# Performance work log

Measured on AMD Instinct MI355X. Metric: run time of the kernel, lower is better.

Reference implementation:

```python
import jax, jax.numpy as jnp
import numpy as np

N = 50000
E = 400000
IN_DIM = 128
HID = 128
OUT = 128
HEADS = 8
NEG_SLOPE = 0.2  # PyG GATConv default
BN_EPS = 1e-5


def _gat_conv(x, W, a_src, a_dst, b, src, dst, concat):
    """PyG GATConv (eval): self-loops added by caller. x:[N,F], W:[F,H*C], a_*:[H,C]."""
    H, C = a_src.shape
    xW = (x @ W).reshape(N, H, C)                       # [N,H,C]
    es = jnp.sum(xW * a_src[None], axis=-1)             # [N,H]
    ed = jnp.sum(xW * a_dst[None], axis=-1)             # [N,H]
    e = jax.nn.leaky_relu(es[src] + ed[dst], NEG_SLOPE) # [E,H]
    m = jax.ops.segment_max(e, dst, num_segments=N)     # softmax over incoming edges per dst
    ex = jnp.exp(e - m[dst])
    denom = jax.ops.segment_sum(ex, dst, num_segments=N)
    alpha = ex / denom[dst]                             # [E,H]
    out = jax.ops.segment_sum(xW[src] * alpha[:, :, None], dst, num_segments=N)  # [N,H,C]
    out = out.reshape(N, H * C) if concat else out.mean(axis=1)
    return out + b


def _bn_eval(h, g, be, rm, rv):
    return (h - rm) * jax.lax.rsqrt(rv + BN_EPS) * g + be


def setup_inputs() -> dict:
    key = jax.random.key(0)
    ks = jax.random.split(key, 20)
    C1 = HID // HEADS
    f32 = jnp.float32
    inp = {
        "x": jax.random.normal(ks[0], (N, IN_DIM), dtype=f32),
        "edge_index": jax.random.randint(ks[1], (2, E), 0, N, dtype=jnp.int64),
        # GAT layer 1 (in->hid, 8 heads, concat)
        "W1": jax.random.normal(ks[2], (IN_DIM, HEADS * C1), dtype=f32) * 0.05,
        "a_src1": jax.random.normal(ks[3], (HEADS, C1), dtype=f32) * 0.05,
        "a_dst1": jax.random.normal(ks[4], (HEADS, C1), dtype=f32) * 0.05,
        "b1": jnp.zeros((HEADS * C1,), dtype=f32),
        # GAT layer 2 (hid->hid, 8 heads, concat)
        "W2": jax.random.normal(ks[5], (HID, HEADS * C1), dtype=f32) * 0.05,
        "a_src2": jax.random.normal(ks[6], (HEADS, C1), dtype=f32) * 0.05,
        "a_dst2": jax.random.normal(ks[7], (HEADS, C1), dtype=f32) * 0.05,
        "b2": jnp.zeros((HEADS * C1,), dtype=f32),
        # GAT layer 3 (hid->out, 1 head, no concat)
        "W3": jax.random.normal(ks[8], (HID, OUT), dtype=f32) * 0.05,
        "a_src3": jax.random.normal(ks[9], (1, OUT), dtype=f32) * 0.05,
        "a_dst3": jax.random.normal(ks[10], (1, OUT), dtype=f32) * 0.05,
        "b3": jnp.zeros((OUT,), dtype=f32),
        # residual linears
        "R1w": jax.random.normal(ks[11], (IN_DIM, HID), dtype=f32) * 0.05,
        "R1b": jnp.zeros((HID,), dtype=f32),
        "R2w": jax.random.normal(ks[12], (HID, HID), dtype=f32) * 0.05,
        "R2b": jnp.zeros((HID,), dtype=f32),
        "R3w": jax.random.normal(ks[13], (HID, OUT), dtype=f32) * 0.05,
        "R3b": jnp.zeros((OUT,), dtype=f32),
        # batch norms (eval mode: running stats)
        "g1": jnp.ones((HID,), dtype=f32), "be1": jnp.zeros((HID,), dtype=f32),
        "rm1": jnp.zeros((HID,), dtype=f32), "rv1": jnp.ones((HID,), dtype=f32),
        "g2": jnp.ones((HID,), dtype=f32), "be2": jnp.zeros((HID,), dtype=f32),
        "rm2": jnp.zeros((HID,), dtype=f32), "rv2": jnp.ones((HID,), dtype=f32),
    }
    return inp


def reference(x, edge_index, W1, a_src1, a_dst1, b1, W2, a_src2, a_dst2, b2,
              W3, a_src3, a_dst3, b3, R1w, R1b, R2w, R2b, R3w, R3b,
              g1, be1, rm1, rv1, g2, be2, rm2, rv2):
    # PyG GATConv adds self-loops by default
    loops = jnp.arange(N, dtype=edge_index.dtype)
    src = jnp.concatenate([edge_index[0], loops])
    dst = jnp.concatenate([edge_index[1], loops])

    h = _gat_conv(x, W1, a_src1, a_dst1, b1, src, dst, concat=True) + (x @ R1w + R1b)
    h1 = jax.nn.relu(_bn_eval(h, g1, be1, rm1, rv1))  # dropout identity in eval

    h = _gat_conv(h1, W2, a_src2, a_dst2, b2, src, dst, concat=True) + (h1 @ R2w + R2b)
    h2 = jax.nn.relu(_bn_eval(h, g2, be2, rm2, rv2))

    out = _gat_conv(h2, W3, a_src3, a_dst3, b3, src, dst, concat=False) + (h2 @ R3w + R3b)
    return out
```

## Files before the change

kernel.cpp:

```cpp
#include <hip/hip_runtime.h>
#include <hip/hip_bf16.h>
#include <type_traits>

typedef __hip_bfloat16 bf16;
typedef __hip_bfloat162 bf162;
typedef short v8s __attribute__((ext_vector_type(8)));
typedef float v4f __attribute__((ext_vector_type(4)));

__device__ __forceinline__ float lrelu(float x) { return x > 0.f ? x : 0.2f * x; }
__device__ __forceinline__ float b2f(bf16 v) { return __bfloat162float(v); }

__global__ void k_count(const int* __restrict__ ei, int* __restrict__ cnt, int E) {
    int i = blockIdx.x * 256 + threadIdx.x;
    if (i < E) atomicAdd(&cnt[ei[E + i]], 1);
}

__global__ void k_scan1(const int* __restrict__ cnt, int* __restrict__ ofs,
                        int* __restrict__ bsum, int n) {
    __shared__ int sh[256];
    int t = threadIdx.x;
    int base = blockIdx.x * 1024 + t * 4;
    int v[4]; int s = 0;
#pragma unroll
    for (int i = 0; i < 4; ++i) { v[i] = (base + i < n) ? cnt[base + i] : 0; s += v[i]; }
    sh[t] = s; __syncthreads();
    for (int o = 1; o < 256; o <<= 1) {
        int x = 0; if (t >= o) x = sh[t - o];
        __syncthreads();
        sh[t] += x;
        __syncthreads();
    }
    int excl = sh[t] - s;
#pragma unroll
    for (int i = 0; i < 4; ++i) { if (base + i < n) ofs[base + i] = excl; excl += v[i]; }
    if (t == 255) bsum[blockIdx.x] = sh[255];
}

__global__ void k_scan2(const int* __restrict__ bsum, int* __restrict__ bpre, int nb) {
    int l = threadIdx.x;
    int v = (l < nb) ? bsum[l] : 0;
    int orig = v;
    for (int o = 1; o < 64; o <<= 1) {
        int x = __shfl_up(v, o);
        if (l >= o) v += x;
    }
    if (l < nb) bpre[l] = v - orig;
}

__global__ void k_scan3(int* __restrict__ ofs, int* __restrict__ cur,
                        const int* __restrict__ bpre, int n) {
    int i = blockIdx.x * 256 + threadIdx.x;
    if (i < n) { int v = ofs[i] + bpre[i >> 10]; ofs[i] = v; cur[i] = v; }
}

__global__ void k_fill(const int* __restrict__ ei, int* __restrict__ cur,
                       int* __restrict__ csr, int E) {
    int i = blockIdx.x * 256 + threadIdx.x;
    if (i < E) {
        int d = ei[E + i];
        int pos = atomicAdd(&cur[d], 1);
        csr[pos] = ei[i];
    }
}

__global__ void k_transpose(const float* __restrict__ s0, const float* __restrict__ s1,
                            const float* __restrict__ s2, const float* __restrict__ s3,
                            const float* __restrict__ s4, const float* __restrict__ s5,
                            bf16* __restrict__ wt) {
    const float* src;
    switch (blockIdx.x) {
        case 0: src = s0; break; case 1: src = s1; break; case 2: src = s2; break;
        case 3: src = s3; break; case 4: src = s4; break; default: src = s5; break;
    }
    bf16* dst = wt + blockIdx.x * 16384;
    for (int i = threadIdx.x; i < 16384; i += 256) {
        int k = i >> 7, n = i & 127;
        dst[n * 128 + k] = __float2bfloat16(src[i]);
    }
}

__global__ void k_params(const float* b1, const float* R1b, const float* g1, const float* be1,
                         const float* rm1, const float* rv1,
                         const float* b2, const float* R2b, const float* g2, const float* be2,
                         const float* rm2, const float* rv2,
                         const float* b3, const float* R3b, float* __restrict__ prm) {
    int c = threadIdx.x;
    if (c < 128) {
        float s1 = g1[c] * rsqrtf(rv1[c] + 1e-5f);
        prm[c]       = b1[c] + R1b[c];
        prm[128 + c] = s1;
        prm[256 + c] = be1[c] - rm1[c] * s1;
        float s2 = g2[c] * rsqrtf(rv2[c] + 1e-5f);
        prm[384 + c] = b2[c] + R2b[c];
        prm[512 + c] = s2;
        prm[640 + c] = be2[c] - rm2[c] * s2;
        prm[768 + c] = b3[c] + R3b[c];
    }
}

template <typename T>
__global__ void gemm_dual(const T* __restrict__ A,
                          const bf16* __restrict__ BT0, const bf16* __restrict__ BT1,
                          bf16* __restrict__ O0, bf16* __restrict__ O1, int nrows) {
    __shared__ bf16 Ash[128 * 128];
    __shared__ bf16 Bsh[128 * 128];
    const bf16* BT = (blockIdx.y == 0) ? BT0 : BT1;
    bf16* O = (blockIdx.y == 0) ? O0 : O1;
    const int t = threadIdx.x;
    const int rowbase = blockIdx.x * 128;
    {
        const int r = t >> 1, hf = t & 1;
        int gr = rowbase + r; if (gr >= nrows) gr = nrows - 1;
        const float4* bsrc = (const float4*)(BT + r * 128 + hf * 64);
        if constexpr (std::is_same<T, float>::value) {
            const float4* asrc = (const float4*)(A + (size_t)gr * 128 + hf * 64);
#pragma unroll
            for (int j = 0; j < 8; ++j) {
                float4 u = asrc[2 * j], w = asrc[2 * j + 1];
                union { bf16 h[8]; float4 f; } tmp;
                tmp.h[0] = __float2bfloat16(u.x); tmp.h[1] = __float2bfloat16(u.y);
                tmp.h[2] = __float2bfloat16(u.z); tmp.h[3] = __float2bfloat16(u.w);
                tmp.h[4] = __float2bfloat16(w.x); tmp.h[5] = __float2bfloat16(w.y);
                tmp.h[6] = __float2bfloat16(w.z); tmp.h[7] = __float2bfloat16(w.w);
                int c = hf * 8 + j, cp = c ^ (r & 7);
                *(float4*)(&Ash[r * 128 + cp * 8]) = tmp.f;
                *(float4*)(&Bsh[r * 128 + cp * 8]) = bsrc[j];
            }
        } else {
            const float4* asrc = (const float4*)(A + (size_t)gr * 128 + hf * 64);
#pragma unroll
            for (int j = 0; j < 8; ++j) {
                int c = hf * 8 + j, cp = c ^ (r & 7);
                *(float4*)(&Ash[r * 128 + cp * 8]) = asrc[j];
                *(float4*)(&Bsh[r * 128 + cp * 8]) = bsrc[j];
            }
        }
    }
    __syncthreads();
    const int wave = t >> 6, lane = t & 63, quad = lane >> 4, l16 = lane & 15;
    v4f acc[2][8];
#pragma unroll
    for (int i = 0; i < 2; ++i)
#pragma unroll
        for (int j = 0; j < 8; ++j) acc[i][j] = (v4f){0.f, 0.f, 0.f, 0.f};
#pragma unroll
    for (int kit = 0; kit < 4; ++kit) {
        v8s afr[2], bfr[8];
#pragma unroll
        for (int rt = 0; rt < 2; ++rt) {
            int row = wave * 32 + rt * 16 + l16;
            int cp = (kit * 4 + quad) ^ (row & 7);
            afr[rt] = *(const v8s*)(&Ash[row * 128 + cp * 8]);
        }
#pragma unroll
        for (int ct = 0; ct < 8; ++ct) {
            int nn = ct * 16 + l16;
            int cp = (kit * 4 + quad) ^ (nn & 7);
            bfr[ct] = *(const v8s*)(&Bsh[nn * 128 + cp * 8]);
        }
#pragma unroll
        for (int rt = 0; rt < 2; ++rt)
#pragma unroll
            for (int ct = 0; ct < 8; ++ct)
                acc[rt][ct] = __builtin_amdgcn_mfma_f32_16x16x32_bf16(afr[rt], bfr[ct], acc[rt][ct], 0, 0, 0);
    }
#pragma unroll
    for (int rt = 0; rt < 2; ++rt)
#pragma unroll
        for (int ct = 0; ct < 8; ++ct)
#pragma unroll
            for (int r = 0; r < 4; ++r) {
                int gr = rowbase + wave * 32 + rt * 16 + quad * 4 + r;
                if (gr < nrows) O[(size_t)gr * 128 + ct * 16 + l16] = __float2bfloat16(acc[rt][ct][r]);
            }
}

__global__ void k_prep8(const bf16* __restrict__ xW, const float* __restrict__ asrc,
                        const float* __restrict__ adst,
                        float* __restrict__ es, float* __restrict__ ed, int n) {
    int wave = threadIdx.x >> 6, lane = threadIdx.x & 63;
    int node = blockIdx.x * 4 + wave;
    if (node >= n) return;
    bf162 xp = *(const bf162*)(xW + (size_t)node * 128 + 2 * lane);
    float2 sp = *(const float2*)(asrc + 2 * lane);
    float2 dp = *(const float2*)(adst + 2 * lane);
    float x0 = b2f(xp.x), x1 = b2f(xp.y);
    float ps = x0 * sp.x + x1 * sp.y;
    float pd = x0 * dp.x + x1 * dp.y;
    for (int o = 1; o < 8; o <<= 1) { ps += __shfl_xor(ps, o); pd += __shfl_xor(pd, o); }
    if ((lane & 7) == 0) {
        int h = lane >> 3;
        es[node * 8 + h] = ps;
        ed[node * 8 + h] = pd;
    }
}

__global__ void k_prep1(const bf16* __restrict__ xW, const float* __restrict__ asrc,
                        const float* __restrict__ adst,
                        float* __restrict__ es, float* __restrict__ ed, int n) {
    int wave = threadIdx.x >> 6, lane = threadIdx.x & 63;
    int node = blockIdx.x * 4 + wave;
    if (node >= n) return;
    bf162 xp = *(const bf162*)(xW + (size_t)node * 128 + 2 * lane);
    float2 sp = *(const float2*)(asrc + 2 * lane);
    float2 dp = *(const float2*)(adst + 2 * lane);
    float x0 = b2f(xp.x), x1 = b2f(xp.y);
    float ps = x0 * sp.x + x1 * sp.y;
    float pd = x0 * dp.x + x1 * dp.y;
    for (int o = 1; o < 64; o <<= 1) { ps += __shfl_xor(ps, o); pd += __shfl_xor(pd, o); }
    if (lane == 0) { es[node] = ps; ed[node] = pd; }
}

__global__ void k_agg8(const bf16* __restrict__ xW, const float* __restrict__ es,
                       const float* __restrict__ ed,
                       const int* __restrict__ ofs, const int* __restrict__ cur,
                       const int* __restrict__ csr,
                       const bf16* __restrict__ rres, const float* __restrict__ prm,
                       bf16* __restrict__ hout, int n) {
    int wave = threadIdx.x >> 6, lane = threadIdx.x & 63;
    int node = blockIdx.x * 4 + wave;
    if (node >= n) return;
    const int g = lane >> 4, l16 = lane & 15;
    const int c0 = l16 * 8;
    const int h = l16 >> 1;
    float edv = ed[node * 8 + h];
    int beg = ofs[node], end = cur[node];
    float acc[8];
    float den = 0.f;
#pragma unroll
    for (int i = 0; i < 8; ++i) acc[i] = 0.f;
    if (g == 0) {
        float ws = __expf(lrelu(es[node * 8 + h] + edv));
        v8s xv = *(const v8s*)(xW + (size_t)node * 128 + c0);
        const bf16* xb = (const bf16*)&xv;
        den = ws;
#pragma unroll
        for (int i = 0; i < 8; ++i) acc[i] = ws * b2f(xb[i]);
    }
    for (int base = beg; base < end; base += 64) {
        int m = end - base; if (m > 64) m = 64;
        int idx = (lane < m) ? csr[base + lane] : node;
        for (int j = 0; j < m; j += 4) {
            int s = __shfl(idx, j + g);
            float e = es[s * 8 + h];
            v8s xv = *(const v8s*)(xW + (size_t)s * 128 + c0);
            float w = ((j + g) < m) ? __expf(lrelu(e + edv)) : 0.f;
            const bf16* xb = (const bf16*)&xv;
            den += w;
#pragma unroll
            for (int i = 0; i < 8; ++i) acc[i] += w * b2f(xb[i]);
        }
    }
    den += __shfl_xor(den, 16); den += __shfl_xor(den, 32);
#pragma unroll
    for (int i = 0; i < 8; ++i) {
        acc[i] += __shfl_xor(acc[i], 16);
        acc[i] += __shfl_xor(acc[i], 32);
    }
    if (g == 0) {
        float inv = 1.f / den;
        v8s rv = *(const v8s*)(rres + (size_t)node * 128 + c0);
        const bf16* rb = (const bf16*)&rv;
        bf16 outv[8];
#pragma unroll
        for (int i = 0; i < 8; ++i) {
            int c = c0 + i;
            float v = acc[i] * inv + prm[c] + b2f(rb[i]);
            v = fmaxf(v * prm[128 + c] + prm[256 + c], 0.f);
            outv[i] = __float2bfloat16(v);
        }
        *(v8s*)(hout + (size_t)node * 128 + c0) = *(v8s*)outv;
    }
}

__global__ void k_agg1(const bf16* __restrict__ xW, const float* __restrict__ es,
                       const float* __restrict__ ed,
                       const int* __restrict__ ofs, const int* __restrict__ cur,
                       const int* __restrict__ csr,
                       const bf16* __restrict__ rres, const float* __restrict__ bias,
                       float* __restrict__ out, int n) {
    int wave = threadIdx.x >> 6, lane = threadIdx.x & 63;
    int node = blockIdx.x * 4 + wave;
    if (node >= n) return;
    const int g = lane >> 4, l16 = lane & 15;
    const int c0 = l16 * 8;
    float edv = ed[node];
    int beg = ofs[node], end = cur[node];
    float acc[8];
    float den = 0.f;
#pragma unroll
    for (int i = 0; i < 8; ++i) acc[i] = 0.f;
    if (g == 0) {
        float ws = __expf(lrelu(es[node] + edv));
        v8s xv = *(const v8s*)(xW + (size_t)node * 128 + c0);
        const bf16* xb = (const bf16*)&xv;
        den = ws;
#pragma unroll
        for (int i = 0; i < 8; ++i) acc[i] = ws * b2f(xb[i]);
    }
    for (int base = beg; base < end; base += 64) {
        int m = end - base; if (m > 64) m = 64;
        int idx = (lane < m) ? csr[base + lane] : node;
        for (int j = 0; j < m; j += 4) {
            int s = __shfl(idx, j + g);
            float e = es[s];
            v8s xv = *(const v8s*)(xW + (size_t)s * 128 + c0);
            float w = ((j + g) < m) ? __expf(lrelu(e + edv)) : 0.f;
            const bf16* xb = (const bf16*)&xv;
            den += w;
#pragma unroll
            for (int i = 0; i < 8; ++i) acc[i] += w * b2f(xb[i]);
        }
    }
    den += __shfl_xor(den, 16); den += __shfl_xor(den, 32);
#pragma unroll
    for (int i = 0; i < 8; ++i) {
        acc[i] += __shfl_xor(acc[i], 16);
        acc[i] += __shfl_xor(acc[i], 32);
    }
    if (g == 0) {
        float inv = 1.f / den;
        v8s rv = *(const v8s*)(rres + (size_t)node * 128 + c0);
        const bf16* rb = (const bf16*)&rv;
        float4 o0, o1;
        float ov[8];
#pragma unroll
        for (int i = 0; i < 8; ++i)
            ov[i] = acc[i] * inv + bias[c0 + i] + b2f(rb[i]);
        o0.x = ov[0]; o0.y = ov[1]; o0.z = ov[2]; o0.w = ov[3];
        o1.x = ov[4]; o1.y = ov[5]; o1.z = ov[6]; o1.w = ov[7];
        *(float4*)(out + (size_t)node * 128 + c0) = o0;
        *(float4*)(out + (size_t)node * 128 + c0 + 4) = o1;
    }
}

extern "C" void kernel_launch(void* const* d_in, const int* in_sizes, int n_in,
                              void* d_out, int out_size, void* d_ws, size_t ws_size,
                              hipStream_t stream) {
    const float* x   = (const float*)d_in[0];
    const int*   ei  = (const int*)d_in[1];
    const float* W1  = (const float*)d_in[2];
    const float* as1 = (const float*)d_in[3];
    const float* ad1 = (const float*)d_in[4];
    const float* b1  = (const float*)d_in[5];
    const float* W2  = (const float*)d_in[6];
    const float* as2 = (const float*)d_in[7];
    const float* ad2 = (const float*)d_in[8];
    const float* b2  = (const float*)d_in[9];
    const float* W3  = (const float*)d_in[10];
    const float* as3 = (const float*)d_in[11];
    const float* ad3 = (const float*)d_in[12];
    const float* b3  = (const float*)d_in[13];
    const float* R1w = (const float*)d_in[14];
    const float* R1b = (const float*)d_in[15];
    const float* R2w = (const float*)d_in[16];
    const float* R2b = (const float*)d_in[17];
    const float* R3w = (const float*)d_in[18];
    const float* R3b = (const float*)d_in[19];
    const float* g1  = (const float*)d_in[20];
    const float* be1 = (const float*)d_in[21];
    const float* rm1 = (const float*)d_in[22];
    const float* rv1 = (const float*)d_in[23];
    const float* g2  = (const float*)d_in[24];
    const float* be2 = (const float*)d_in[25];
    const float* rm2 = (const float*)d_in[26];
    const float* rv2 = (const float*)d_in[27];

    const int N = in_sizes[0] / 128;
    const int E = in_sizes[1] / 2;

    char* p = (char*)d_ws;
    size_t off = 0;
    auto alloc = [&](size_t b) { void* r = p + off; off = (off + b + 255) & ~(size_t)255; return r; };
    int*   cnt  = (int*)alloc((size_t)N * 4);
    int*   ofs  = (int*)alloc((size_t)N * 4);
    int*   cur  = (int*)alloc((size_t)N * 4);
    int*   bsum = (int*)alloc(64 * 4);
    int*   bpre = (int*)alloc(64 * 4);
    int*   csr  = (int*)alloc((size_t)E * 4);
    bf16*  WT   = (bf16*)alloc((size_t)6 * 16384 * 2);
    float* prm  = (float*)alloc(896 * 4);
    float* es   = (float*)alloc((size_t)N * 8 * 4);
    float* ed   = (float*)alloc((size_t)N * 8 * 4);
    bf16*  xW   = (bf16*)alloc((size_t)N * 128 * 2);
    bf16*  rres = (bf16*)alloc((size_t)N * 128 * 2);
    bf16*  hA   = (bf16*)alloc((size_t)N * 128 * 2);
    bf16*  hB   = (bf16*)alloc((size_t)N * 128 * 2);
    (void)ws_size; (void)n_in; (void)out_size;

    hipMemsetAsync(cnt, 0, (size_t)N * 4, stream);
    const int eb = (E + 255) / 256;
    const int nb = (N + 1023) / 1024;
    k_count<<<eb, 256, 0, stream>>>(ei, cnt, E);
    k_scan1<<<nb, 256, 0, stream>>>(cnt, ofs, bsum, N);
    k_scan2<<<1, 64, 0, stream>>>(bsum, bpre, nb);
    k_scan3<<<(N + 255) / 256, 256, 0, stream>>>(ofs, cur, bpre, N);
    k_fill<<<eb, 256, 0, stream>>>(ei, cur, csr, E);
    k_transpose<<<6, 256, 0, stream>>>(W1, R1w, W2, R2w, W3, R3w, WT);
    k_params<<<1, 128, 0, stream>>>(b1, R1b, g1, be1, rm1, rv1,
                                    b2, R2b, g2, be2, rm2, rv2, b3, R3b, prm);

    const int gx = (N + 127) / 128;
    const int nw = (N + 3) / 4;
    gemm_dual<float><<<dim3(gx, 2), 256, 0, stream>>>(x, WT, WT + 16384, xW, rres, N);
    k_prep8<<<nw, 256, 0, stream>>>(xW, as1, ad1, es, ed, N);
    k_agg8<<<nw, 256, 0, stream>>>(xW, es, ed, ofs, cur, csr, rres, prm, hA, N);
    gemm_dual<bf16><<<dim3(gx, 2), 256, 0, stream>>>(hA, WT + 2 * 16384, WT + 3 * 16384, xW, rres, N);
    k_prep8<<<nw, 256, 0, stream>>>(xW, as2, ad2, es, ed, N);
    k_agg8<<<nw, 256, 0, stream>>>(xW, es, ed, ofs, cur, csr, rres, prm + 384, hB, N);
    gemm_dual<bf16><<<dim3(gx, 2), 256, 0, stream>>>(hB, WT + 4 * 16384, WT + 5 * 16384, xW, rres, N);
    k_prep1<<<nw, 256, 0, stream>>>(xW, as3, ad3, es, ed, N);
    k_agg1<<<nw, 256, 0, stream>>>(xW, es, ed, ofs, cur, csr, rres, prm + 768, (float*)d_out, N);
}
```

Before: 350.2 us.

## Fold attention logits into GEMM as extra weight columns; dedupe edge exp work

```diff
diff --git a/kernel.cpp b/kernel.cpp
--- a/kernel.cpp
+++ b/kernel.cpp
@@ -63,47 +63,83 @@
     }
 }
 
-__global__ void k_transpose(const float* __restrict__ s0, const float* __restrict__ s1,
-                            const float* __restrict__ s2, const float* __restrict__ s3,
-                            const float* __restrict__ s4, const float* __restrict__ s5,
-                            bf16* __restrict__ wt) {
+__global__ void k_trans(const float* __restrict__ s0, const float* __restrict__ s1,
+                        const float* __restrict__ s2, const float* __restrict__ s3,
+                        const float* __restrict__ s4, const float* __restrict__ s5,
+                        const float* __restrict__ as1, const float* __restrict__ ad1,
+                        const float* __restrict__ as2, const float* __restrict__ ad2,
+                        const float* __restrict__ as3, const float* __restrict__ ad3,
+                        const float* b1, const float* R1b, const float* g1, const float* be1,
+                        const float* rm1, const float* rv1,
+                        const float* b2, const float* R2b, const float* g2, const float* be2,
+                        const float* rm2, const float* rv2,
+                        const float* b3, const float* R3b,
+                        bf16* __restrict__ wt, float* __restrict__ prm) {
+    int b = blockIdx.x;
+    int t = threadIdx.x;
+    if (b == 6) {
+        int c = t;
+        if (c < 128) {
+            float s1v = g1[c] * rsqrtf(rv1[c] + 1e-5f);
+            prm[c]       = b1[c] + R1b[c];
+            prm[128 + c] = s1v;
+            prm[256 + c] = be1[c] - rm1[c] * s1v;
+            float s2v = g2[c] * rsqrtf(rv2[c] + 1e-5f);
+            prm[384 + c] = b2[c] + R2b[c];
+            prm[512 + c] = s2v;
+            prm[640 + c] = be2[c] - rm2[c] * s2v;
+            prm[768 + c] = b3[c] + R3b[c];
+        }
+        return;
+    }
     const float* src;
-    switch (blockIdx.x) {
+    switch (b) {
         case 0: src = s0; break; case 1: src = s1; break; case 2: src = s2; break;
         case 3: src = s3; break; case 4: src = s4; break; default: src = s5; break;
     }
-    bf16* dst = wt + blockIdx.x * 16384;
-    for (int i = threadIdx.x; i < 16384; i += 256) {
+    bf16* dst = wt + (size_t)b * 18432;
+    for (int i = t; i < 16384; i += 256) {
         int k = i >> 7, n = i & 127;
         dst[n * 128 + k] = __float2bfloat16(src[i]);
     }
-}
-
-__global__ void k_params(const float* b1, const float* R1b, const float* g1, const float* be1,
-                         const float* rm1, const float* rv1,
-                         const float* b2, const float* R2b, const float* g2, const float* be2,
-                         const float* rm2, const float* rv2,
-                         const float* b3, const float* R3b, float* __restrict__ prm) {
-    int c = threadIdx.x;
-    if (c < 128) {
-        float s1 = g1[c] * rsqrtf(rv1[c] + 1e-5f);
-        prm[c]       = b1[c] + R1b[c];
-        prm[128 + c] = s1;
-        prm[256 + c] = be1[c] - rm1[c] * s1;
-        float s2 = g2[c] * rsqrtf(rv2[c] + 1e-5f);
-        prm[384 + c] = b2[c] + R2b[c];
-        prm[512 + c] = s2;
-        prm[640 + c] = be2[c] - rm2[c] * s2;
-        prm[768 + c] = b3[c] + R3b[c];
+    if ((b & 1) == 0) {
+        int layer = b >> 1;
+        if (layer < 2) {
+            const float* asr = (layer == 0) ? as1 : as2;
+            const float* ads = (layer == 0) ? ad1 : ad2;
+            for (int i = t; i < 2048; i += 256) {
+                int row = i >> 7, k = i & 127, h = row & 7;
+                const float* av = (row < 8) ? asr : ads;
+                float s = 0.f;
+#pragma unroll
+                for (int c = 0; c < 16; ++c) s += src[k * 128 + h * 16 + c] * av[h * 16 + c];
+                dst[(128 + row) * 128 + k] = __float2bfloat16(s);
+            }
+        } else {
+            for (int i = t; i < 2048; i += 256) {
+                int row = i >> 7, k = i & 127;
+                float s = 0.f;
+                if (row == 0 || row == 8) {
+                    const float* av = (row == 0) ? as3 : ad3;
+                    for (int c = 0; c < 128; ++c) s += src[k * 128 + c] * av[c];
+                }
+                dst[(128 + row) * 128 + k] = __float2bfloat16(s);
+            }
+        }
+    } else {
+        for (int i = t; i < 2048; i += 256)
+            dst[16384 + i] = __float2bfloat16(0.f);
     }
 }
 
 template <typename T>
 __global__ void gemm_dual(const T* __restrict__ A,
                           const bf16* __restrict__ BT0, const bf16* __restrict__ BT1,
-                          bf16* __restrict__ O0, bf16* __restrict__ O1, int nrows) {
+                          bf16* __restrict__ O0, bf16* __restrict__ O1,
+                          float* __restrict__ es, float* __restrict__ ed,
+                          int mode, int nrows) {
     __shared__ bf16 Ash[128 * 128];
-    __shared__ bf16 Bsh[128 * 128];
+    __shared__ bf16 Bsh[144 * 128];
     const bf16* BT = (blockIdx.y == 0) ? BT0 : BT1;
     bf16* O = (blockIdx.y == 0) ? O0 : O1;
     const int t = threadIdx.x;
@@ -111,7 +147,6 @@
     {
         const int r = t >> 1, hf = t & 1;
         int gr = rowbase + r; if (gr >= nrows) gr = nrows - 1;
-        const float4* bsrc = (const float4*)(BT + r * 128 + hf * 64);
         if constexpr (std::is_same<T, float>::value) {
             const float4* asrc = (const float4*)(A + (size_t)gr * 128 + hf * 64);
 #pragma unroll
@@ -124,7 +159,6 @@
                 tmp.h[6] = __float2bfloat16(w.z); tmp.h[7] = __float2bfloat16(w.w);
                 int c = hf * 8 + j, cp = c ^ (r & 7);
                 *(float4*)(&Ash[r * 128 + cp * 8]) = tmp.f;
-                *(float4*)(&Bsh[r * 128 + cp * 8]) = bsrc[j];
             }
         } else {
             const float4* asrc = (const float4*)(A + (size_t)gr * 128 + hf * 64);
@@ -132,20 +166,28 @@
             for (int j = 0; j < 8; ++j) {
                 int c = hf * 8 + j, cp = c ^ (r & 7);
                 *(float4*)(&Ash[r * 128 + cp * 8]) = asrc[j];
-                *(float4*)(&Bsh[r * 128 + cp * 8]) = bsrc[j];
-            }
+            }
+        }
+    }
+    for (int s = t; s < 288; s += 256) {
+        int r = s >> 1, hf = s & 1;
+        const float4* bsrc = (const float4*)(BT + r * 128 + hf * 64);
+#pragma unroll
+        for (int j = 0; j < 8; ++j) {
+            int c = hf * 8 + j, cp = c ^ (r & 7);
+            *(float4*)(&Bsh[r * 128 + cp * 8]) = bsrc[j];
         }
     }
     __syncthreads();
     const int wave = t >> 6, lane = t & 63, quad = lane >> 4, l16 = lane & 15;
-    v4f acc[2][8];
+    v4f acc[2][9];
 #pragma unroll
     for (int i = 0; i < 2; ++i)
 #pragma unroll
-        for (int j = 0; j < 8; ++j) acc[i][j] = (v4f){0.f, 0.f, 0.f, 0.f};
+        for (int j = 0; j < 9; ++j) acc[i][j] = (v4f){0.f, 0.f, 0.f, 0.f};
 #pragma unroll
     for (int kit = 0; kit < 4; ++kit) {
-        v8s afr[2], bfr[8];
+        v8s afr[2], bfr[9];
 #pragma unroll
         for (int rt = 0; rt < 2; ++rt) {
             int row = wave * 32 + rt * 16 + l16;
@@ -153,7 +195,7 @@
             afr[rt] = *(const v8s*)(&Ash[row * 128 + cp * 8]);
         }
 #pragma unroll
-        for (int ct = 0; ct < 8; ++ct) {
+        for (int ct = 0; ct < 9; ++ct) {
             int nn = ct * 16 + l16;
             int cp = (kit * 4 + quad) ^ (nn & 7);
             bfr[ct] = *(const v8s*)(&Bsh[nn * 128 + cp * 8]);
@@ -161,7 +203,7 @@
 #pragma unroll
         for (int rt = 0; rt < 2; ++rt)
 #pragma unroll
-            for (int ct = 0; ct < 8; ++ct)
+            for (int ct = 0; ct < 9; ++ct)
                 acc[rt][ct] = __builtin_amdgcn_mfma_f32_16x16x32_bf16(afr[rt], bfr[ct], acc[rt][ct], 0, 0, 0);
     }
 #pragma unroll
@@ -173,46 +215,28 @@
                 int gr = rowbase + wave * 32 + rt * 16 + quad * 4 + r;
                 if (gr < nrows) O[(size_t)gr * 128 + ct * 16 + l16] = __float2bfloat16(acc[rt][ct][r]);
             }
-}
-
-__global__ void k_prep8(const bf16* __restrict__ xW, const float* __restrict__ asrc,
-                        const float* __restrict__ adst,
-                        float* __restrict__ es, float* __restrict__ ed, int n) {
-    int wave = threadIdx.x >> 6, lane = threadIdx.x & 63;
-    int node = blockIdx.x * 4 + wave;
-    if (node >= n) return;
-    bf162 xp = *(const bf162*)(xW + (size_t)node * 128 + 2 * lane);
-    float2 sp = *(const float2*)(asrc + 2 * lane);
-    float2 dp = *(const float2*)(adst + 2 * lane);
-    float x0 = b2f(xp.x), x1 = b2f(xp.y);
-    float ps = x0 * sp.x + x1 * sp.y;
-    float pd = x0 * dp.x + x1 * dp.y;
-    for (int o = 1; o < 8; o <<= 1) { ps += __shfl_xor(ps, o); pd += __shfl_xor(pd, o); }
-    if ((lane & 7) == 0) {
-        int h = lane >> 3;
-        es[node * 8 + h] = ps;
-        ed[node * 8 + h] = pd;
-    }
-}
-
-__global__ void k_prep1(const bf16* __restrict__ xW, const float* __restrict__ asrc,
-                        const float* __restrict__ adst,
-                        float* __restrict__ es, float* __restrict__ ed, int n) {
-    int wave = threadIdx.x >> 6, lane = threadIdx.x & 63;
-    int node = blockIdx.x * 4 + wave;
-    if (node >= n) return;
-    bf162 xp = *(const bf162*)(xW + (size_t)node * 128 + 2 * lane);
-    float2 sp = *(const float2*)(asrc + 2 * lane);
-    float2 dp = *(const float2*)(adst + 2 * lane);
-    float x0 = b2f(xp.x), x1 = b2f(xp.y);
-    float ps = x0 * sp.x + x1 * sp.y;
-    float pd = x0 * dp.x + x1 * dp.y;
-    for (int o = 1; o < 64; o <<= 1) { ps += __shfl_xor(ps, o); pd += __shfl_xor(pd, o); }
-    if (lane == 0) { es[node] = ps; ed[node] = pd; }
-}
-
-__global__ void k_agg8(const bf16* __restrict__ xW, const float* __restrict__ es,
-                       const float* __restrict__ ed,
+    if (mode != 0 && blockIdx.y == 0) {
+#pragma unroll
+        for (int rt = 0; rt < 2; ++rt)
+#pragma unroll
+            for (int r = 0; r < 4; ++r) {
+                int gr = rowbase + wave * 32 + rt * 16 + quad * 4 + r;
+                if (gr < nrows) {
+                    float v = acc[rt][8][r];
+                    if (mode == 1) {
+                        if (l16 < 8) es[(size_t)gr * 8 + l16] = v;
+                        else         ed[(size_t)gr * 8 + (l16 - 8)] = v;
+                    } else {
+                        if (l16 == 0) es[gr] = v;
+                        else if (l16 == 8) ed[gr] = v;
+                    }
+                }
+            }
+    }
+}
+
+__global__ void k_agg8(const bf16* __restrict__ xW, const float* __restrict__ es8,
+                       const float* __restrict__ ed8,
                        const int* __restrict__ ofs, const int* __restrict__ cur,
                        const int* __restrict__ csr,
                        const bf16* __restrict__ rres, const float* __restrict__ prm,
@@ -222,33 +246,44 @@
     if (node >= n) return;
     const int g = lane >> 4, l16 = lane & 15;
     const int c0 = l16 * 8;
-    const int h = l16 >> 1;
-    float edv = ed[node * 8 + h];
+    const int hc = l16 >> 1;
+    const int he = lane & 7;
+    float edw = ed8[(size_t)node * 8 + he];
+    float wselfh = __expf(lrelu(es8[(size_t)node * 8 + he] + edw));
+    float acc[8]; float den = 0.f;
+#pragma unroll
+    for (int i = 0; i < 8; ++i) acc[i] = 0.f;
+    {
+        float ws = __shfl(wselfh, hc);
+        if (g == 0) {
+            v8s xv = *(const v8s*)(xW + (size_t)node * 128 + c0);
+            const bf16* xb = (const bf16*)&xv;
+            den = ws;
+#pragma unroll
+            for (int i = 0; i < 8; ++i) acc[i] = ws * b2f(xb[i]);
+        }
+    }
     int beg = ofs[node], end = cur[node];
-    float acc[8];
-    float den = 0.f;
-#pragma unroll
-    for (int i = 0; i < 8; ++i) acc[i] = 0.f;
-    if (g == 0) {
-        float ws = __expf(lrelu(es[node * 8 + h] + edv));
-        v8s xv = *(const v8s*)(xW + (size_t)node * 128 + c0);
-        const bf16* xb = (const bf16*)&xv;
-        den = ws;
-#pragma unroll
-        for (int i = 0; i < 8; ++i) acc[i] = ws * b2f(xb[i]);
-    }
     for (int base = beg; base < end; base += 64) {
         int m = end - base; if (m > 64) m = 64;
         int idx = (lane < m) ? csr[base + lane] : node;
-        for (int j = 0; j < m; j += 4) {
-            int s = __shfl(idx, j + g);
-            float e = es[s * 8 + h];
-            v8s xv = *(const v8s*)(xW + (size_t)s * 128 + c0);
-            float w = ((j + g) < m) ? __expf(lrelu(e + edv)) : 0.f;
-            const bf16* xb = (const bf16*)&xv;
-            den += w;
-#pragma unroll
-            for (int i = 0; i < 8; ++i) acc[i] += w * b2f(xb[i]);
+        for (int sub = 0; sub * 8 < m; ++sub) {
+            int e = sub * 8 + (lane >> 3);
+            int sidx = __shfl(idx, e & 63);
+            float esv = es8[(size_t)sidx * 8 + he];
+            float w = (e < m) ? __expf(lrelu(esv + edw)) : 0.f;
+#pragma unroll
+            for (int jj = 0; jj < 2; ++jj) {
+                int jo = jj * 4 + g;
+                int j = sub * 8 + jo;
+                int sv = __shfl(idx, j & 63);
+                float wj = __shfl(w, jo * 8 + hc);
+                v8s xv = *(const v8s*)(xW + (size_t)sv * 128 + c0);
+                const bf16* xb = (const bf16*)&xv;
+                den += wj;
+#pragma unroll
+                for (int i = 0; i < 8; ++i) acc[i] += wj * b2f(xb[i]);
+            }
         }
     }
     den += __shfl_xor(den, 16); den += __shfl_xor(den, 32);
@@ -285,31 +320,32 @@
     const int g = lane >> 4, l16 = lane & 15;
     const int c0 = l16 * 8;
     float edv = ed[node];
-    int beg = ofs[node], end = cur[node];
-    float acc[8];
-    float den = 0.f;
+    float wself = __expf(lrelu(es[node] + edv));
+    float acc[8]; float den = 0.f;
 #pragma unroll
     for (int i = 0; i < 8; ++i) acc[i] = 0.f;
     if (g == 0) {
-        float ws = __expf(lrelu(es[node] + edv));
         v8s xv = *(const v8s*)(xW + (size_t)node * 128 + c0);
         const bf16* xb = (const bf16*)&xv;
-        den = ws;
-#pragma unroll
-        for (int i = 0; i < 8; ++i) acc[i] = ws * b2f(xb[i]);
-    }
+        den = wself;
+#pragma unroll
+        for (int i = 0; i < 8; ++i) acc[i] = wself * b2f(xb[i]);
+    }
+    int beg = ofs[node], end = cur[node];
     for (int base = beg; base < end; base += 64) {
         int m = end - base; if (m > 64) m = 64;
         int idx = (lane < m) ? csr[base + lane] : node;
+        float w = (lane < m) ? __expf(lrelu(es[idx] + edv)) : 0.f;
         for (int j = 0; j < m; j += 4) {
-            int s = __shfl(idx, j + g);
-            float e = es[s];
-            v8s xv = *(const v8s*)(xW + (size_t)s * 128 + c0);
-            float w = ((j + g) < m) ? __expf(lrelu(e + edv)) : 0.f;
+            int jl = j + g;
+            int sv = __shfl(idx, jl & 63);
+            float wj = __shfl(w, jl & 63);
+            if (jl >= m) wj = 0.f;
+            v8s xv = *(const v8s*)(xW + (size_t)sv * 128 + c0);
             const bf16* xb = (const bf16*)&xv;
-            den += w;
-#pragma unroll
-            for (int i = 0; i < 8; ++i) acc[i] += w * b2f(xb[i]);
+            den += wj;
+#pragma unroll
+            for (int i = 0; i < 8; ++i) acc[i] += wj * b2f(xb[i]);
         }
     }
     den += __shfl_xor(den, 16); den += __shfl_xor(den, 32);
@@ -322,11 +358,11 @@
         float inv = 1.f / den;
         v8s rv = *(const v8s*)(rres + (size_t)node * 128 + c0);
         const bf16* rb = (const bf16*)&rv;
-        float4 o0, o1;
         float ov[8];
 #pragma unroll
         for (int i = 0; i < 8; ++i)
             ov[i] = acc[i] * inv + bias[c0 + i] + b2f(rb[i]);
+        float4 o0, o1;
         o0.x = ov[0]; o0.y = ov[1]; o0.z = ov[2]; o0.w = ov[3];
         o1.x = ov[4]; o1.y = ov[5]; o1.z = ov[6]; o1.w = ov[7];
         *(float4*)(out + (size_t)node * 128 + c0) = o0;
@@ -378,7 +414,7 @@
     int*   bsum = (int*)alloc(64 * 4);
     int*   bpre = (int*)alloc(64 * 4);
     int*   csr  = (int*)alloc((size_t)E * 4);
-    bf16*  WT   = (bf16*)alloc((size_t)6 * 16384 * 2);
+    bf16*  WT   = (bf16*)alloc((size_t)6 * 18432 * 2);
     float* prm  = (float*)alloc(896 * 4);
     float* es   = (float*)alloc((size_t)N * 8 * 4);
     float* ed   = (float*)alloc((size_t)N * 8 * 4);
@@ -396,19 +432,18 @@
     k_scan2<<<1, 64, 0, stream>>>(bsum, bpre, nb);
     k_scan3<<<(N + 255) / 256, 256, 0, stream>>>(ofs, cur, bpre, N);
     k_fill<<<eb, 256, 0, stream>>>(ei, cur, csr, E);
-    k_transpose<<<6, 256, 0, stream>>>(W1, R1w, W2, R2w, W3, R3w, WT);
-    k_params<<<1, 128, 0, stream>>>(b1, R1b, g1, be1, rm1, rv1,
-                                    b2, R2b, g2, be2, rm2, rv2, b3, R3b, prm);
+    k_trans<<<7, 256, 0, stream>>>(W1, R1w, W2, R2w, W3, R3w,
+                                   as1, ad1, as2, ad2, as3, ad3,
+                                   b1, R1b, g1, be1, rm1, rv1,
+                                   b2, R2b, g2, be2, rm2, rv2, b3, R3b,
+                                   WT, prm);
 
     const int gx = (N + 127) / 128;
     const int nw = (N + 3) / 4;
-    gemm_dual<float><<<dim3(gx, 2), 256, 0, stream>>>(x, WT, WT + 16384, xW, rres, N);
-    k_prep8<<<nw, 256, 0, stream>>>(xW, as1, ad1, es, ed, N);
+    gemm_dual<float><<<dim3(gx, 2), 256, 0, stream>>>(x, WT, WT + 18432, xW, rres, es, ed, 1, N);
     k_agg8<<<nw, 256, 0, stream>>>(xW, es, ed, ofs, cur, csr, rres, prm, hA, N);
-    gemm_dual<bf16><<<dim3(gx, 2), 256, 0, stream>>>(hA, WT + 2 * 16384, WT + 3 * 16384, xW, rres, N);
-    k_prep8<<<nw, 256, 0, stream>>>(xW, as2, ad2, es, ed, N);
+    gemm_dual<bf16><<<dim3(gx, 2), 256, 0, stream>>>(hA, WT + 2 * 18432, WT + 3 * 18432, xW, rres, es, ed, 1, N);
     k_agg8<<<nw, 256, 0, stream>>>(xW, es, ed, ofs, cur, csr, rres, prm + 384, hB, N);
-    gemm_dual<bf16><<<dim3(gx, 2), 256, 0, stream>>>(hB, WT + 4 * 16384, WT + 5 * 16384, xW, rres, N);
-    k_prep1<<<nw, 256, 0, stream>>>(xW, as3, ad3, es, ed, N);
+    gemm_dual<bf16><<<dim3(gx, 2), 256, 0, stream>>>(hB, WT + 4 * 18432, WT + 5 * 18432, xW, rres, es, ed, 2, N);
     k_agg1<<<nw, 256, 0, stream>>>(xW, es, ed, ofs, cur, csr, rres, prm + 768, (float*)d_out, N);
 }
```

After: 346.7 us. About the same (-1.0%).
